# Kernel optimization log

Measured on AMD Instinct MI355X. Metric: run time of the kernel, lower is better.

Reference implementation:

```python
import jax, jax.numpy as jnp
import numpy as np


def setup_inputs() -> dict:
    key = jax.random.key(0)
    k1, k2 = jax.random.split(key)
    x = jax.random.normal(k1, (32, 256, 32, 32), dtype=jnp.float32)
    emb = jax.random.uniform(k2, (256, 2048), dtype=jnp.float32)
    return {"x": x, "emb": emb}


def reference(x, emb):
    # x: (B, D, H, W), emb: (D, K)
    B, D = x.shape[0], x.shape[1]
    spatial = x.shape[2:]
    K = emb.shape[1]
    # flatten latents: (N, D) with N = B*H*W
    xf = jnp.moveaxis(x, 1, -1).reshape(-1, D)
    d2 = (jnp.sum(xf * xf, axis=-1, keepdims=True)
          - 2.0 * (xf @ emb)
          + jnp.sum(emb * emb, axis=0))  # (N, K)
    argmin = jnp.argmin(d2, axis=-1)  # (N,)
    q = jnp.take(emb.T, argmin, axis=0)  # (N, D) nearest codes
    out = q.reshape(B, *spatial, D)
    out = jnp.moveaxis(out, -1, 1)  # (B, D, H, W)
    return out
```

## Files before the change

kernel.cpp:

```cpp
#include <hip/hip_runtime.h>


typedef __attribute__((ext_vector_type(8))) _Float16 half8v;
typedef __attribute__((ext_vector_type(16))) float floatx16;
typedef unsigned int uint;
typedef unsigned short ushort;

#define DD 256
#define KK 2048
#define SS 1024
#define NN 32768
#define MT 128
#define NTT 256
#define LDA 24
#define MFMA_F16 __builtin_amdgcn_mfma_f32_32x32x16_f16

#define XSLAB  262144
#define XPLANE 131072
#define EPLANE 262144

union HU { _Float16 f; ushort u; };

__device__ __forceinline__ void split16(float v, ushort& h, ushort& l) {
    HU a, b;
    a.f = (_Float16)v;
    b.f = (_Float16)(v - (float)a.f);
    h = a.u; l = b.u;
}

__global__ __launch_bounds__(256) void hn_kernel(const float* __restrict__ emb,
                                                 float* __restrict__ hn) {
    int k = blockIdx.x * 256 + threadIdx.x;
    float a = 0.f;
#pragma unroll 32
    for (int d = 0; d < DD; ++d) { float e = emb[d * KK + k]; a += e * e; }
    hn[k] = 0.5f * a;
}

__global__ __launch_bounds__(256) void pack_emb(const float* __restrict__ emb,
                                                uint* __restrict__ epk) {
    int idx = blockIdx.x * 256 + threadIdx.x;
    int k = idx & (KK - 1);
    int d2 = idx >> 11;
    float a = emb[(size_t)(2 * d2) * KK + k];
    float b = emb[(size_t)(2 * d2 + 1) * KK + k];
    ushort h0, l0, h1, l1;
    split16(a, h0, l0);
    split16(b, h1, l1);
    epk[idx] = (uint)h0 | ((uint)h1 << 16);
    epk[EPLANE + idx] = (uint)l0 | ((uint)l1 << 16);
}

__global__ __launch_bounds__(256) void pack_x(const float* __restrict__ x,
                                              uint* __restrict__ px) {
    int idx = blockIdx.x * 256 + threadIdx.x;
    int s4 = idx & 255;
    int d2 = (idx >> 8) & 127;
    int bq = idx >> 15;
    const float4* xp = reinterpret_cast<const float4*>(
        x + ((size_t)(bq * DD + 2 * d2)) * SS) + s4;
    float4 a = xp[0];
    float4 b = xp[SS / 4];
    ushort h0, l0, h1, l1;
    uint4 th, tl;
    split16(a.x, h0, l0); split16(b.x, h1, l1);
    th.x = (uint)h0 | ((uint)h1 << 16); tl.x = (uint)l0 | ((uint)l1 << 16);
    split16(a.y, h0, l0); split16(b.y, h1, l1);
    th.y = (uint)h0 | ((uint)h1 << 16); tl.y = (uint)l0 | ((uint)l1 << 16);
    split16(a.z, h0, l0); split16(b.z, h1, l1);
    th.z = (uint)h0 | ((uint)h1 << 16); tl.z = (uint)l0 | ((uint)l1 << 16);
    split16(a.w, h0, l0); split16(b.w, h1, l1);
    th.w = (uint)h0 | ((uint)h1 << 16); tl.w = (uint)l0 | ((uint)l1 << 16);
    size_t o4 = (size_t)bq * (XSLAB / 4) + (size_t)d2 * (SS / 4) + s4;
    reinterpret_cast<uint4*>(px)[o4] = th;
    reinterpret_cast<uint4*>(px)[o4 + XPLANE / 4] = tl;
}

template <bool PRE>
__global__ __launch_bounds__(512, 1) void vq_fused(
        const float* __restrict__ x, const float* __restrict__ emb,
        const float* __restrict__ hn, const uint* __restrict__ epk,
        float* out) {
    __shared__ ushort Ah[2][MT * LDA], Al[2][MT * LDA];
    __shared__ ushort Bh[2][NTT * LDA], Bl[2][NTT * LDA];
    __shared__ float sv[4][MT];
    __shared__ int   sc[4][MT];
    __shared__ int   bc[MT];

    const int tid = threadIdx.x;
    const int lane = tid & 63;
    const int wid = tid >> 6;
    const int colk = lane & 31;
    const int half = lane >> 5;
    const int wm = (wid & 1) * 64;
    const int wn = (wid >> 1) * 64;

    const int base_n = blockIdx.x * MT;
    const int bq = base_n >> 10;
    const int sb = base_n & (SS - 1);

    const int lat_a = tid & 127;
    const int dqa = (tid >> 7) * 4;
    const int cod_b = tid & 255;
    const int dqb = (tid >> 8) * 8;

    const float* xb = x + ((size_t)bq * DD + dqa) * SS + sb + lat_a;
    const uint* aH = reinterpret_cast<const uint*>(out)
                     + (size_t)bq * XSLAB + (size_t)(dqa >> 1) * SS + sb + lat_a;
    const uint* eH = epk + (size_t)(dqb >> 1) * KK + cod_b;

    floatx16 acc[2][2];
#pragma unroll
    for (int i = 0; i < 2; ++i)
#pragma unroll
        for (int j = 0; j < 2; ++j) acc[i][j] = (floatx16)(0.0f);

    float bestv[2][16];
    int bestc[2][16];
#pragma unroll
    for (int t = 0; t < 2; ++t)
#pragma unroll
        for (int r = 0; r < 16; ++r) { bestv[t][r] = 3.4e38f; bestc[t][r] = 0; }

    float fa[4], fb[8];
    uint ua[4], ub[8];
    if constexpr (PRE) {
#pragma unroll
        for (int i = 0; i < 2; ++i) {
            ua[i] = aH[(size_t)i * SS];
            ua[2 + i] = aH[XPLANE + (size_t)i * SS];
        }
#pragma unroll
        for (int i = 0; i < 4; ++i) {
            ub[i] = eH[(size_t)i * KK];
            ub[4 + i] = eH[EPLANE + (size_t)i * KK];
        }
    } else {
#pragma unroll
        for (int i = 0; i < 4; ++i) fa[i] = xb[(size_t)i * SS];
        const float* p = emb + (size_t)dqb * KK + cod_b;
#pragma unroll
        for (int i = 0; i < 8; ++i) fb[i] = p[(size_t)i * KK];
    }
    if constexpr (PRE) {
        uint2 w; uint4 t;
        w.x = ua[0]; w.y = ua[1];
        *reinterpret_cast<uint2*>(&Ah[0][lat_a * LDA + dqa]) = w;
        w.x = ua[2]; w.y = ua[3];
        *reinterpret_cast<uint2*>(&Al[0][lat_a * LDA + dqa]) = w;
        t.x = ub[0]; t.y = ub[1]; t.z = ub[2]; t.w = ub[3];
        *reinterpret_cast<uint4*>(&Bh[0][cod_b * LDA + dqb]) = t;
        t.x = ub[4]; t.y = ub[5]; t.z = ub[6]; t.w = ub[7];
        *reinterpret_cast<uint4*>(&Bl[0][cod_b * LDA + dqb]) = t;
    } else {
        ushort h[8], l[8];
#pragma unroll
        for (int i = 0; i < 4; ++i) split16(fa[i], h[i], l[i]);
        uint2 w;
        w.x = (uint)h[0] | ((uint)h[1] << 16);
        w.y = (uint)h[2] | ((uint)h[3] << 16);
        *reinterpret_cast<uint2*>(&Ah[0][lat_a * LDA + dqa]) = w;
        w.x = (uint)l[0] | ((uint)l[1] << 16);
        w.y = (uint)l[2] | ((uint)l[3] << 16);
        *reinterpret_cast<uint2*>(&Al[0][lat_a * LDA + dqa]) = w;
#pragma unroll
        for (int i = 0; i < 8; ++i) split16(fb[i], h[i], l[i]);
        uint4 t;
        t.x = (uint)h[0] | ((uint)h[1] << 16);
        t.y = (uint)h[2] | ((uint)h[3] << 16);
        t.z = (uint)h[4] | ((uint)h[5] << 16);
        t.w = (uint)h[6] | ((uint)h[7] << 16);
        *reinterpret_cast<uint4*>(&Bh[0][cod_b * LDA + dqb]) = t;
        t.x = (uint)l[0] | ((uint)l[1] << 16);
        t.y = (uint)l[2] | ((uint)l[3] << 16);
        t.z = (uint)l[4] | ((uint)l[5] << 16);
        t.w = (uint)l[6] | ((uint)l[7] << 16);
        *reinterpret_cast<uint4*>(&Bl[0][cod_b * LDA + dqb]) = t;
    }
    __syncthreads();

    for (int c = 0; c < 128; ++c) {
        const int cur = c & 1, nxt = cur ^ 1;
        if (c < 127) {
            const int c1 = c + 1;
            const int kt1 = c1 >> 4;
            const int dt1 = (c1 & 15) * 16;
            if constexpr (PRE) {
                const uint* pa = aH + (size_t)(dt1 >> 1) * SS;
#pragma unroll
                for (int i = 0; i < 2; ++i) {
                    ua[i] = pa[(size_t)i * SS];
                    ua[2 + i] = pa[XPLANE + (size_t)i * SS];
                }
                const uint* pb = eH + (size_t)(dt1 >> 1) * KK + kt1 * NTT;
#pragma unroll
                for (int i = 0; i < 4; ++i) {
                    ub[i] = pb[(size_t)i * KK];
                    ub[4 + i] = pb[EPLANE + (size_t)i * KK];
                }
            } else {
#pragma unroll
                for (int i = 0; i < 4; ++i) fa[i] = xb[(size_t)(dt1 + i) * SS];
                const float* p = emb + (size_t)(dt1 + dqb) * KK + kt1 * NTT + cod_b;
#pragma unroll
                for (int i = 0; i < 8; ++i) fb[i] = p[(size_t)i * KK];
            }
        }
        const int fo = colk * LDA + half * 8;
        half8v ah0 = *reinterpret_cast<const half8v*>(&Ah[cur][fo + wm * LDA]);
        half8v ah1 = *reinterpret_cast<const half8v*>(&Ah[cur][fo + (wm + 32) * LDA]);
        half8v al0 = *reinterpret_cast<const half8v*>(&Al[cur][fo + wm * LDA]);
        half8v al1 = *reinterpret_cast<const half8v*>(&Al[cur][fo + (wm + 32) * LDA]);
        half8v bh0 = *reinterpret_cast<const half8v*>(&Bh[cur][fo + wn * LDA]);
        half8v bh1 = *reinterpret_cast<const half8v*>(&Bh[cur][fo + (wn + 32) * LDA]);
        half8v bl0 = *reinterpret_cast<const half8v*>(&Bl[cur][fo + wn * LDA]);
        half8v bl1 = *reinterpret_cast<const half8v*>(&Bl[cur][fo + (wn + 32) * LDA]);

        acc[0][0] = MFMA_F16(ah0, bh0, acc[0][0], 0, 0, 0);
        acc[0][0] = MFMA_F16(ah0, bl0, acc[0][0], 0, 0, 0);
        acc[0][0] = MFMA_F16(al0, bh0, acc[0][0], 0, 0, 0);

        acc[0][1] = MFMA_F16(ah0, bh1, acc[0][1], 0, 0, 0);
        acc[0][1] = MFMA_F16(ah0, bl1, acc[0][1], 0, 0, 0);
        acc[0][1] = MFMA_F16(al0, bh1, acc[0][1], 0, 0, 0);

        acc[1][0] = MFMA_F16(ah1, bh0, acc[1][0], 0, 0, 0);
        acc[1][0] = MFMA_F16(ah1, bl0, acc[1][0], 0, 0, 0);
        acc[1][0] = MFMA_F16(al1, bh0, acc[1][0], 0, 0, 0);

        acc[1][1] = MFMA_F16(ah1, bh1, acc[1][1], 0, 0, 0);
        acc[1][1] = MFMA_F16(ah1, bl1, acc[1][1], 0, 0, 0);
        acc[1][1] = MFMA_F16(al1, bh1, acc[1][1], 0, 0, 0);

        if (c < 127) {
            if constexpr (PRE) {
                uint2 w; uint4 t;
                w.x = ua[0]; w.y = ua[1];
                *reinterpret_cast<uint2*>(&Ah[nxt][lat_a * LDA + dqa]) = w;
                w.x = ua[2]; w.y = ua[3];
                *reinterpret_cast<uint2*>(&Al[nxt][lat_a * LDA + dqa]) = w;
                t.x = ub[0]; t.y = ub[1]; t.z = ub[2]; t.w = ub[3];
                *reinterpret_cast<uint4*>(&Bh[nxt][cod_b * LDA + dqb]) = t;
                t.x = ub[4]; t.y = ub[5]; t.z = ub[6]; t.w = ub[7];
                *reinterpret_cast<uint4*>(&Bl[nxt][cod_b * LDA + dqb]) = t;
            } else {
                ushort h[8], l[8];
#pragma unroll
                for (int i = 0; i < 4; ++i) split16(fa[i], h[i], l[i]);
                uint2 w;
                w.x = (uint)h[0] | ((uint)h[1] << 16);
                w.y = (uint)h[2] | ((uint)h[3] << 16);
                *reinterpret_cast<uint2*>(&Ah[nxt][lat_a * LDA + dqa]) = w;
                w.x = (uint)l[0] | ((uint)l[1] << 16);
                w.y = (uint)l[2] | ((uint)l[3] << 16);
                *reinterpret_cast<uint2*>(&Al[nxt][lat_a * LDA + dqa]) = w;
#pragma unroll
                for (int i = 0; i < 8; ++i) split16(fb[i], h[i], l[i]);
                uint4 t;
                t.x = (uint)h[0] | ((uint)h[1] << 16);
                t.y = (uint)h[2] | ((uint)h[3] << 16);
                t.z = (uint)h[4] | ((uint)h[5] << 16);
                t.w = (uint)h[6] | ((uint)h[7] << 16);
                *reinterpret_cast<uint4*>(&Bh[nxt][cod_b * LDA + dqb]) = t;
                t.x = (uint)l[0] | ((uint)l[1] << 16);
                t.y = (uint)l[2] | ((uint)l[3] << 16);
                t.z = (uint)l[4] | ((uint)l[5] << 16);
                t.w = (uint)l[6] | ((uint)l[7] << 16);
                *reinterpret_cast<uint4*>(&Bl[nxt][cod_b * LDA + dqb]) = t;
            }
        }
        if ((c & 15) == 15) {
            const int kt = c >> 4;
            const int cd0 = kt * NTT + wn + colk;
            const int cd1 = cd0 + 32;
            const float h0 = hn[cd0];
            const float h1 = hn[cd1];
#pragma unroll
            for (int tm = 0; tm < 2; ++tm) {
#pragma unroll
                for (int r = 0; r < 16; ++r) {
                    float s0 = h0 - acc[tm][0][r];
                    float s1 = h1 - acc[tm][1][r];
                    float v = s0; int cd = cd0;
                    if (s1 < s0) { v = s1; cd = cd1; }
                    if (v < bestv[tm][r]) { bestv[tm][r] = v; bestc[tm][r] = cd; }
                    acc[tm][0][r] = 0.f;
                    acc[tm][1][r] = 0.f;
                }
            }
        }
        __syncthreads();
    }

#pragma unroll
    for (int tm = 0; tm < 2; ++tm) {
#pragma unroll
        for (int r = 0; r < 16; ++r) {
            float v = bestv[tm][r];
            int cd = bestc[tm][r];
#pragma unroll
            for (int mk = 1; mk < 32; mk <<= 1) {
                float ov = __shfl_xor(v, mk);
                int oc = __shfl_xor(cd, mk);
                if (ov < v || (ov == v && oc < cd)) { v = ov; cd = oc; }
            }
            if (colk == 0) {
                const int row = (r & 3) + 8 * (r >> 2) + 4 * half;
                sv[wid >> 1][wm + tm * 32 + row] = v;
                sc[wid >> 1][wm + tm * 32 + row] = cd;
            }
        }
    }
    __syncthreads();
    if (tid < MT) {
        float v = sv[0][tid]; int cd = sc[0][tid];
#pragma unroll
        for (int g = 1; g < 4; ++g) {
            float ov = sv[g][tid]; int oc = sc[g][tid];
            if (ov < v || (ov == v && oc < cd)) { v = ov; cd = oc; }
        }
        bc[tid] = cd;
    }
    __syncthreads();
    {
        const int mq = tid & 31;
        const int dg = tid >> 5;
        const int k0 = bc[mq * 4 + 0];
        const int k1 = bc[mq * 4 + 1];
        const int k2 = bc[mq * 4 + 2];
        const int k3 = bc[mq * 4 + 3];
#pragma unroll 4
        for (int dd = 0; dd < 16; ++dd) {
            const int d = dg * 16 + dd;
            const float* er = emb + (size_t)d * KK;
            float4 o = make_float4(er[k0], er[k1], er[k2], er[k3]);
            reinterpret_cast<float4*>(&out[((size_t)bq * DD + d) * SS + sb])[mq] = o;
        }
    }
}

extern "C" void kernel_launch(void* const* d_in, const int* in_sizes, int n_in,
                              void* d_out, int out_size, void* d_ws, size_t ws_size,
                              hipStream_t stream) {
    const float* x = (const float*)d_in[0];
    const float* emb = (const float*)d_in[1];
    float* out = (float*)d_out;
    float* hn = (float*)d_ws;
    uint* epk = (uint*)((char*)d_ws + KK * sizeof(float));

    const size_t need = (size_t)KK * 4 + (size_t)2 * EPLANE * 4;

    hipLaunchKernelGGL(hn_kernel, dim3(KK / 256), dim3(256), 0, stream, emb, hn);
    if (ws_size >= need) {
        hipLaunchKernelGGL(pack_emb, dim3(EPLANE / 256), dim3(256), 0, stream,
                           emb, epk);
        hipLaunchKernelGGL(pack_x, dim3(4096), dim3(256), 0, stream,
                           x, (uint*)out);
        hipLaunchKernelGGL((vq_fused<true>), dim3(NN / MT), dim3(512), 0, stream,
                           x, emb, hn, epk, out);
    } else {
        hipLaunchKernelGGL((vq_fused<false>), dim3(NN / MT), dim3(512), 0, stream,
                           x, emb, hn, epk, out);
    }
}
```

Baseline: 255.4 us.

## Halve latent tile to 64 rows and raise occupancy to four blocks per CU

Shrinks the per-block latent tile from 128 to 64 rows, so each warp computes one 32-row MFMA tile instead of two. The A-tile load, the argmin reduction and the gather/writeback are reindexed to match. Launch bounds change to allow up to four blocks per CU, aiming for more resident waves and a larger grid to hide memory latency. In exchange each block re-streams the full codebook for half as many latents, doubling codebook global/LDS traffic per output, and the MFMA-to-load ratio per barrier drops.

```diff
diff --git a/kernel.cpp b/kernel.cpp
--- a/kernel.cpp
+++ b/kernel.cpp
@@ -10,7 +10,7 @@
 #define KK 2048
 #define SS 1024
 #define NN 32768
-#define MT 128
+#define MT 64
 #define NTT 256
 #define LDA 24
 #define MFMA_F16 __builtin_amdgcn_mfma_f32_32x32x16_f16
@@ -77,7 +77,7 @@
 }
 
 template <bool PRE>
-__global__ __launch_bounds__(512, 1) void vq_fused(
+__global__ __launch_bounds__(512, 4) void vq_fused(
         const float* __restrict__ x, const float* __restrict__ emb,
         const float* __restrict__ hn, const uint* __restrict__ epk,
         float* out) {
@@ -92,77 +92,66 @@
     const int wid = tid >> 6;
     const int colk = lane & 31;
     const int half = lane >> 5;
-    const int wm = (wid & 1) * 64;
+    const int wm = (wid & 1) * 32;
     const int wn = (wid >> 1) * 64;
 
     const int base_n = blockIdx.x * MT;
     const int bq = base_n >> 10;
     const int sb = base_n & (SS - 1);
 
-    const int lat_a = tid & 127;
-    const int dqa = (tid >> 7) * 4;
+    const int lat_a = tid & 63;
+    const int dqa2 = tid >> 6;
     const int cod_b = tid & 255;
     const int dqb = (tid >> 8) * 8;
-
-    const float* xb = x + ((size_t)bq * DD + dqa) * SS + sb + lat_a;
+    const int dqb2 = (tid >> 8) * 4;
+
+    const float* xb = x + ((size_t)bq * DD + 2 * dqa2) * SS + sb + lat_a;
     const uint* aH = reinterpret_cast<const uint*>(out)
-                     + (size_t)bq * XSLAB + (size_t)(dqa >> 1) * SS + sb + lat_a;
-    const uint* eH = epk + (size_t)(dqb >> 1) * KK + cod_b;
-
-    floatx16 acc[2][2];
-#pragma unroll
-    for (int i = 0; i < 2; ++i)
-#pragma unroll
-        for (int j = 0; j < 2; ++j) acc[i][j] = (floatx16)(0.0f);
-
-    float bestv[2][16];
-    int bestc[2][16];
-#pragma unroll
-    for (int t = 0; t < 2; ++t)
-#pragma unroll
-        for (int r = 0; r < 16; ++r) { bestv[t][r] = 3.4e38f; bestc[t][r] = 0; }
-
-    float fa[4], fb[8];
-    uint ua[4], ub[8];
+                     + (size_t)bq * XSLAB + (size_t)dqa2 * SS + sb + lat_a;
+    const uint* eH = epk + (size_t)dqb2 * KK + cod_b;
+
+    floatx16 acc[2];
+#pragma unroll
+    for (int j = 0; j < 2; ++j) acc[j] = (floatx16)(0.0f);
+
+    float bestv[16];
+    int bestc[16];
+#pragma unroll
+    for (int r = 0; r < 16; ++r) { bestv[r] = 3.4e38f; bestc[r] = 0; }
+
+    float fa[2], fb[8];
+    uint ua[2], ub[8];
     if constexpr (PRE) {
-#pragma unroll
-        for (int i = 0; i < 2; ++i) {
-            ua[i] = aH[(size_t)i * SS];
-            ua[2 + i] = aH[XPLANE + (size_t)i * SS];
-        }
+        ua[0] = aH[0];
+        ua[1] = aH[XPLANE];
 #pragma unroll
         for (int i = 0; i < 4; ++i) {
             ub[i] = eH[(size_t)i * KK];
             ub[4 + i] = eH[EPLANE + (size_t)i * KK];
         }
     } else {
-#pragma unroll
-        for (int i = 0; i < 4; ++i) fa[i] = xb[(size_t)i * SS];
+        fa[0] = xb[0];
+        fa[1] = xb[SS];
         const float* p = emb + (size_t)dqb * KK + cod_b;
 #pragma unroll
         for (int i = 0; i < 8; ++i) fb[i] = p[(size_t)i * KK];
     }
     if constexpr (PRE) {
-        uint2 w; uint4 t;
-        w.x = ua[0]; w.y = ua[1];
-        *reinterpret_cast<uint2*>(&Ah[0][lat_a * LDA + dqa]) = w;
-        w.x = ua[2]; w.y = ua[3];
-        *reinterpret_cast<uint2*>(&Al[0][lat_a * LDA + dqa]) = w;
+        *reinterpret_cast<uint*>(&Ah[0][lat_a * LDA + dqa2 * 2]) = ua[0];
+        *reinterpret_cast<uint*>(&Al[0][lat_a * LDA + dqa2 * 2]) = ua[1];
+        uint4 t;
         t.x = ub[0]; t.y = ub[1]; t.z = ub[2]; t.w = ub[3];
         *reinterpret_cast<uint4*>(&Bh[0][cod_b * LDA + dqb]) = t;
         t.x = ub[4]; t.y = ub[5]; t.z = ub[6]; t.w = ub[7];
         *reinterpret_cast<uint4*>(&Bl[0][cod_b * LDA + dqb]) = t;
     } else {
         ushort h[8], l[8];
-#pragma unroll
-        for (int i = 0; i < 4; ++i) split16(fa[i], h[i], l[i]);
-        uint2 w;
-        w.x = (uint)h[0] | ((uint)h[1] << 16);
-        w.y = (uint)h[2] | ((uint)h[3] << 16);
-        *reinterpret_cast<uint2*>(&Ah[0][lat_a * LDA + dqa]) = w;
-        w.x = (uint)l[0] | ((uint)l[1] << 16);
-        w.y = (uint)l[2] | ((uint)l[3] << 16);
-        *reinterpret_cast<uint2*>(&Al[0][lat_a * LDA + dqa]) = w;
+        split16(fa[0], h[0], l[0]);
+        split16(fa[1], h[1], l[1]);
+        *reinterpret_cast<uint*>(&Ah[0][lat_a * LDA + dqa2 * 2]) =
+            (uint)h[0] | ((uint)h[1] << 16);
+        *reinterpret_cast<uint*>(&Al[0][lat_a * LDA + dqa2 * 2]) =
+            (uint)l[0] | ((uint)l[1] << 16);
 #pragma unroll
         for (int i = 0; i < 8; ++i) split16(fb[i], h[i], l[i]);
         uint4 t;
@@ -187,11 +176,8 @@
             const int dt1 = (c1 & 15) * 16;
             if constexpr (PRE) {
                 const uint* pa = aH + (size_t)(dt1 >> 1) * SS;
-#pragma unroll
-                for (int i = 0; i < 2; ++i) {
-                    ua[i] = pa[(size_t)i * SS];
-                    ua[2 + i] = pa[XPLANE + (size_t)i * SS];
-                }
+                ua[0] = pa[0];
+                ua[1] = pa[XPLANE];
                 const uint* pb = eH + (size_t)(dt1 >> 1) * KK + kt1 * NTT;
 #pragma unroll
                 for (int i = 0; i < 4; ++i) {
@@ -199,61 +185,46 @@
                     ub[4 + i] = pb[EPLANE + (size_t)i * KK];
                 }
             } else {
-#pragma unroll
-                for (int i = 0; i < 4; ++i) fa[i] = xb[(size_t)(dt1 + i) * SS];
+                fa[0] = xb[(size_t)dt1 * SS];
+                fa[1] = xb[(size_t)dt1 * SS + SS];
                 const float* p = emb + (size_t)(dt1 + dqb) * KK + kt1 * NTT + cod_b;
 #pragma unroll
                 for (int i = 0; i < 8; ++i) fb[i] = p[(size_t)i * KK];
             }
         }
         const int fo = colk * LDA + half * 8;
-        half8v ah0 = *reinterpret_cast<const half8v*>(&Ah[cur][fo + wm * LDA]);
-        half8v ah1 = *reinterpret_cast<const half8v*>(&Ah[cur][fo + (wm + 32) * LDA]);
-        half8v al0 = *reinterpret_cast<const half8v*>(&Al[cur][fo + wm * LDA]);
-        half8v al1 = *reinterpret_cast<const half8v*>(&Al[cur][fo + (wm + 32) * LDA]);
+        half8v ah = *reinterpret_cast<const half8v*>(&Ah[cur][fo + wm * LDA]);
+        half8v al = *reinterpret_cast<const half8v*>(&Al[cur][fo + wm * LDA]);
         half8v bh0 = *reinterpret_cast<const half8v*>(&Bh[cur][fo + wn * LDA]);
         half8v bh1 = *reinterpret_cast<const half8v*>(&Bh[cur][fo + (wn + 32) * LDA]);
         half8v bl0 = *reinterpret_cast<const half8v*>(&Bl[cur][fo + wn * LDA]);
         half8v bl1 = *reinterpret_cast<const half8v*>(&Bl[cur][fo + (wn + 32) * LDA]);
 
-        acc[0][0] = MFMA_F16(ah0, bh0, acc[0][0], 0, 0, 0);
-        acc[0][0] = MFMA_F16(ah0, bl0, acc[0][0], 0, 0, 0);
-        acc[0][0] = MFMA_F16(al0, bh0, acc[0][0], 0, 0, 0);
-
-        acc[0][1] = MFMA_F16(ah0, bh1, acc[0][1], 0, 0, 0);
-        acc[0][1] = MFMA_F16(ah0, bl1, acc[0][1], 0, 0, 0);
-        acc[0][1] = MFMA_F16(al0, bh1, acc[0][1], 0, 0, 0);
-
-        acc[1][0] = MFMA_F16(ah1, bh0, acc[1][0], 0, 0, 0);
-        acc[1][0] = MFMA_F16(ah1, bl0, acc[1][0], 0, 0, 0);
-        acc[1][0] = MFMA_F16(al1, bh0, acc[1][0], 0, 0, 0);
-
-        acc[1][1] = MFMA_F16(ah1, bh1, acc[1][1], 0, 0, 0);
-        acc[1][1] = MFMA_F16(ah1, bl1, acc[1][1], 0, 0, 0);
-        acc[1][1] = MFMA_F16(al1, bh1, acc[1][1], 0, 0, 0);
+        acc[0] = MFMA_F16(ah, bh0, acc[0], 0, 0, 0);
+        acc[0] = MFMA_F16(ah, bl0, acc[0], 0, 0, 0);
+        acc[0] = MFMA_F16(al, bh0, acc[0], 0, 0, 0);
+
+        acc[1] = MFMA_F16(ah, bh1, acc[1], 0, 0, 0);
+        acc[1] = MFMA_F16(ah, bl1, acc[1], 0, 0, 0);
+        acc[1] = MFMA_F16(al, bh1, acc[1], 0, 0, 0);
 
         if (c < 127) {
             if constexpr (PRE) {
-                uint2 w; uint4 t;
-                w.x = ua[0]; w.y = ua[1];
-                *reinterpret_cast<uint2*>(&Ah[nxt][lat_a * LDA + dqa]) = w;
-                w.x = ua[2]; w.y = ua[3];
-                *reinterpret_cast<uint2*>(&Al[nxt][lat_a * LDA + dqa]) = w;
+                *reinterpret_cast<uint*>(&Ah[nxt][lat_a * LDA + dqa2 * 2]) = ua[0];
+                *reinterpret_cast<uint*>(&Al[nxt][lat_a * LDA + dqa2 * 2]) = ua[1];
+                uint4 t;
                 t.x = ub[0]; t.y = ub[1]; t.z = ub[2]; t.w = ub[3];
                 *reinterpret_cast<uint4*>(&Bh[nxt][cod_b * LDA + dqb]) = t;
                 t.x = ub[4]; t.y = ub[5]; t.z = ub[6]; t.w = ub[7];
                 *reinterpret_cast<uint4*>(&Bl[nxt][cod_b * LDA + dqb]) = t;
             } else {
                 ushort h[8], l[8];
-#pragma unroll
-                for (int i = 0; i < 4; ++i) split16(fa[i], h[i], l[i]);
-                uint2 w;
-                w.x = (uint)h[0] | ((uint)h[1] << 16);
-                w.y = (uint)h[2] | ((uint)h[3] << 16);
-                *reinterpret_cast<uint2*>(&Ah[nxt][lat_a * LDA + dqa]) = w;
-                w.x = (uint)l[0] | ((uint)l[1] << 16);
-                w.y = (uint)l[2] | ((uint)l[3] << 16);
-                *reinterpret_cast<uint2*>(&Al[nxt][lat_a * LDA + dqa]) = w;
+                split16(fa[0], h[0], l[0]);
+                split16(fa[1], h[1], l[1]);
+                *reinterpret_cast<uint*>(&Ah[nxt][lat_a * LDA + dqa2 * 2]) =
+                    (uint)h[0] | ((uint)h[1] << 16);
+                *reinterpret_cast<uint*>(&Al[nxt][lat_a * LDA + dqa2 * 2]) =
+                    (uint)l[0] | ((uint)l[1] << 16);
 #pragma unroll
                 for (int i = 0; i < 8; ++i) split16(fb[i], h[i], l[i]);
                 uint4 t;
@@ -276,39 +247,33 @@
             const float h0 = hn[cd0];
             const float h1 = hn[cd1];
 #pragma unroll
-            for (int tm = 0; tm < 2; ++tm) {
-#pragma unroll
-                for (int r = 0; r < 16; ++r) {
-                    float s0 = h0 - acc[tm][0][r];
-                    float s1 = h1 - acc[tm][1][r];
-                    float v = s0; int cd = cd0;
-                    if (s1 < s0) { v = s1; cd = cd1; }
-                    if (v < bestv[tm][r]) { bestv[tm][r] = v; bestc[tm][r] = cd; }
-                    acc[tm][0][r] = 0.f;
-                    acc[tm][1][r] = 0.f;
-                }
+            for (int r = 0; r < 16; ++r) {
+                float s0 = h0 - acc[0][r];
+                float s1 = h1 - acc[1][r];
+                float v = s0; int cd = cd0;
+                if (s1 < s0) { v = s1; cd = cd1; }
+                if (v < bestv[r]) { bestv[r] = v; bestc[r] = cd; }
+                acc[0][r] = 0.f;
+                acc[1][r] = 0.f;
             }
         }
         __syncthreads();
     }
 
 #pragma unroll
-    for (int tm = 0; tm < 2; ++tm) {
-#pragma unroll
-        for (int r = 0; r < 16; ++r) {
-            float v = bestv[tm][r];
-            int cd = bestc[tm][r];
-#pragma unroll
-            for (int mk = 1; mk < 32; mk <<= 1) {
-                float ov = __shfl_xor(v, mk);
-                int oc = __shfl_xor(cd, mk);
-                if (ov < v || (ov == v && oc < cd)) { v = ov; cd = oc; }
-            }
-            if (colk == 0) {
-                const int row = (r & 3) + 8 * (r >> 2) + 4 * half;
-                sv[wid >> 1][wm + tm * 32 + row] = v;
-                sc[wid >> 1][wm + tm * 32 + row] = cd;
-            }
+    for (int r = 0; r < 16; ++r) {
+        float v = bestv[r];
+        int cd = bestc[r];
+#pragma unroll
+        for (int mk = 1; mk < 32; mk <<= 1) {
+            float ov = __shfl_xor(v, mk);
+            int oc = __shfl_xor(cd, mk);
+            if (ov < v || (ov == v && oc < cd)) { v = ov; cd = oc; }
+        }
+        if (colk == 0) {
+            const int row = (r & 3) + 8 * (r >> 2) + 4 * half;
+            sv[wid >> 1][wm + row] = v;
+            sc[wid >> 1][wm + row] = cd;
         }
     }
     __syncthreads();
@@ -323,15 +288,15 @@
     }
     __syncthreads();
     {
-        const int mq = tid & 31;
-        const int dg = tid >> 5;
+        const int mq = tid & 15;
+        const int dg = tid >> 4;
         const int k0 = bc[mq * 4 + 0];
         const int k1 = bc[mq * 4 + 1];
         const int k2 = bc[mq * 4 + 2];
         const int k3 = bc[mq * 4 + 3];
 #pragma unroll 4
-        for (int dd = 0; dd < 16; ++dd) {
-            const int d = dg * 16 + dd;
+        for (int dd = 0; dd < 8; ++dd) {
+            const int d = dg * 8 + dd;
             const float* er = emb + (size_t)d * KK;
             float4 o = make_float4(er[k0], er[k1], er[k2], er[k3]);
             reinterpret_cast<float4*>(&out[((size_t)bq * DD + d) * SS + sb])[mq] = o;
```

Measured after the change: 262.3 us. 1.03x slower.
